# Kernel optimization log

Hardware: AMD Instinct MI355X
Metric: run time of the kernel (lower is better)

Reference implementation:

```python
import math
import jax, jax.numpy as jnp
import numpy as np

D_MODEL = 1024
N_HEADS = 16
D_K = D_MODEL // N_HEADS


def setup_inputs() -> dict:
    key = jax.random.key(0)
    ks = jax.random.split(key, 10)
    s = 1.0 / math.sqrt(D_MODEL)
    return {
        "x": jax.random.normal(ks[0], (4, 4096, D_MODEL), dtype=jnp.float32),
        "memory_key": jax.random.normal(ks[1], (4, 4096, D_MODEL), dtype=jnp.float32),
        "Wq": jax.random.normal(ks[2], (D_MODEL, D_MODEL), dtype=jnp.float32) * s,
        "bq": jnp.zeros((D_MODEL,), dtype=jnp.float32),
        "Wk": jax.random.normal(ks[3], (D_MODEL, D_MODEL), dtype=jnp.float32) * s,
        "bk": jnp.zeros((D_MODEL,), dtype=jnp.float32),
        "Wv": jax.random.normal(ks[4], (D_MODEL, D_MODEL), dtype=jnp.float32) * s,
        "bv": jnp.zeros((D_MODEL,), dtype=jnp.float32),
        "Wo": jax.random.normal(ks[5], (D_MODEL, D_MODEL), dtype=jnp.float32) * s,
        "bo": jnp.zeros((D_MODEL,), dtype=jnp.float32),
    }


def _heads(t, b, n):
    # [b, n, d_model] -> [b, h, n, d_k]
    return t.reshape(b, n, N_HEADS, D_K).transpose(0, 2, 1, 3)


def reference(x, memory_key, Wq, bq, Wk, bk, Wv, bv, Wo, bo):
    b, n, _ = x.shape
    scale = 1.0 / math.sqrt(D_K)
    q = _heads(x @ Wq + bq, b, n)
    k = _heads(x @ Wk + bk, b, n)
    v = _heads(x @ Wv + bv, b, n)
    # feature-dim softmax (over d_k), scaled by 1/sqrt(d_k)
    q_soft = jax.nn.softmax(q * scale, axis=-1)
    k_soft = jax.nn.softmax(k * scale, axis=-1)
    kv = jnp.einsum('bhnd,bhne->bhde', k_soft, v)   # [b,h,d_k,d_k]
    out = jnp.einsum('bhnd,bhde->bhne', q_soft, kv)
    # memory path: softmax over reshaped memory_key heads, same value tensor
    m_soft = jax.nn.softmax(_heads(memory_key, b, n) * scale, axis=-1)
    mv = jnp.einsum('bhnd,bhne->bhde', m_soft, v)
    out = out + jnp.einsum('bhnd,bhde->bhne', q_soft, mv)
    out = out.transpose(0, 2, 1, 3).reshape(b, n, D_MODEL)
    # dropout is identity in eval mode
    return out @ Wo + bo
```

## Files before the change

### kernel.cpp

```cpp
#include <hip/hip_runtime.h>
#include <stdint.h>

typedef unsigned int uint;
typedef unsigned short ushort;
typedef __attribute__((ext_vector_type(4))) float  f32x4;
typedef __attribute__((ext_vector_type(8))) __bf16 bf16x8;

#define SCALE 0.125f

__device__ __forceinline__ ushort f2bf(float f) {
  uint u = __builtin_bit_cast(uint, f);
  u += 0x7FFFu + ((u >> 16) & 1u);
  return (ushort)(u >> 16);
}
__device__ __forceinline__ uint pack2bf(float a, float b) {
  return (uint)f2bf(a) | ((uint)f2bf(b) << 16);
}
__device__ __forceinline__ float bflo(uint u) { return __builtin_bit_cast(float, u << 16); }
__device__ __forceinline__ float bfhi(uint u) { return __builtin_bit_cast(float, u & 0xFFFF0000u); }

__device__ __forceinline__ void gload_lds16(const void* g, void* l) {
  __builtin_amdgcn_global_load_lds((const __attribute__((address_space(1))) void*)g,
                                   (__attribute__((address_space(3))) void*)l, 16, 0, 0);
}

__device__ __forceinline__ void unpack8(uint4 u, float s, float* x) {
  x[0]=bflo(u.x)*s; x[1]=bfhi(u.x)*s; x[2]=bflo(u.y)*s; x[3]=bfhi(u.y)*s;
  x[4]=bflo(u.z)*s; x[5]=bfhi(u.z)*s; x[6]=bflo(u.w)*s; x[7]=bfhi(u.w)*s;
}


__global__ __launch_bounds__(256) void cvt_all_kernel(
    const float4* __restrict__ x, uint2* __restrict__ xb,
    const float* __restrict__ Wq, const float* __restrict__ Wk, const float* __restrict__ Wv,
    ushort* __restrict__ WT, float4* __restrict__ S4) {
  __shared__ float tile[32][33];
  int bx = blockIdx.x;
  if (bx < 2048) {
    int i = bx * 256 + threadIdx.x;
    #pragma unroll
    for (int k = 0; k < 8; ++k) {
      int idx = i + k * 524288;
      float4 f = x[idx];
      xb[idx] = make_uint2(pack2bf(f.x, f.y), pack2bf(f.z, f.w));
    }
  } else if (bx < 5120) {
    int lin = bx - 2048;
    int mat = lin >> 10;
    int rem = lin & 1023;
    int cb = rem & 31, rb = rem >> 5;
    const float* W = (mat == 0) ? Wq : (mat == 1) ? Wk : Wv;
    int tx = threadIdx.x & 31, ty = threadIdx.x >> 5;
    int c0 = cb * 32, r0 = rb * 32;
    #pragma unroll
    for (int i = 0; i < 4; ++i)
      tile[ty + i*8][tx] = W[(size_t)(r0 + ty + i*8) * 1024 + c0 + tx];
    __syncthreads();
    #pragma unroll
    for (int i = 0; i < 4; ++i)
      WT[(size_t)(mat*1024 + c0 + ty + i*8) * 1024 + r0 + tx] = f2bf(tile[tx][ty + i*8]);
  } else {
    int base = ((bx - 5120) * 256 + threadIdx.x) * 8;
    const float4 z = {0.f, 0.f, 0.f, 0.f};
    #pragma unroll
    for (int j = 0; j < 8; ++j) S4[base + j] = z;
  }
}


__global__ __launch_bounds__(256, 2) void gemm1_qkv(
    const ushort* __restrict__ A, const ushort* __restrict__ B,
    ushort* __restrict__ QKV, ushort* __restrict__ qs,
    const float* __restrict__ bq, const float* __restrict__ bk, const float* __restrict__ bv) {
  __shared__ ushort As[128 * 64];
  __shared__ ushort Bs[128 * 64];
  const int K = 1024;
  const int t = threadIdx.x;
  const int w = t >> 6, l = t & 63;
  const int wr = w >> 1, wc = w & 1;
  const int m0 = blockIdx.x * 128;
  const int n0 = blockIdx.y * 128;
  const ushort* Ap = A + (size_t)m0 * K;
  const ushort* Bp = B + (size_t)n0 * K;

  f32x4 acc[4][4];
  const f32x4 zf = {0.f, 0.f, 0.f, 0.f};
  #pragma unroll
  for (int i = 0; i < 4; ++i)
    #pragma unroll
    for (int j = 0; j < 4; ++j) acc[i][j] = zf;

  const int lr = l & 15, lg = l >> 4;

  for (int kt = 0; kt < K; kt += 64) {
    #pragma unroll
    for (int i = 0; i < 4; ++i) {
      int gb = w * 64 + i * 256;
      int g  = gb + l;
      int row = g >> 3, c16 = g & 7;
      gload_lds16(Ap + (size_t)row * K + kt + c16 * 8, (void*)(As + gb * 8));
      gload_lds16(Bp + (size_t)row * K + kt + c16 * 8, (void*)(Bs + gb * 8));
    }
    __syncthreads();
    #pragma unroll
    for (int kk = 0; kk < 64; kk += 32) {
      bf16x8 a[4], b[4];
      #pragma unroll
      for (int m = 0; m < 4; ++m)
        a[m] = *(const bf16x8*)(As + (wr*64 + m*16 + lr) * 64 + kk + lg * 8);
      #pragma unroll
      for (int n = 0; n < 4; ++n)
        b[n] = *(const bf16x8*)(Bs + (wc*64 + n*16 + lr) * 64 + kk + lg * 8);
      #pragma unroll
      for (int m = 0; m < 4; ++m)
        #pragma unroll
        for (int n = 0; n < 4; ++n)
          acc[m][n] = __builtin_amdgcn_mfma_f32_16x16x32_bf16(a[m], b[n], acc[m][n], 0, 0, 0);
    }
    __syncthreads();
  }

  if (n0 < 1024) {
    const int cb = n0 + wc * 64;
    float bvv[4];
    #pragma unroll
    for (int n = 0; n < 4; ++n) bvv[n] = bq[cb + n*16 + lr];
    #pragma unroll
    for (int m = 0; m < 4; ++m) {
      #pragma unroll
      for (int j = 0; j < 4; ++j) {
        int row = m0 + wr*64 + m*16 + lg*4 + j;
        float v[4];
        float s = 0.f;
        #pragma unroll
        for (int n = 0; n < 4; ++n) {
          v[n] = __expf((acc[m][n][j] + bvv[n]) * SCALE);
          s += v[n];
        }
        s += __shfl_xor(s, 1);
        s += __shfl_xor(s, 2);
        s += __shfl_xor(s, 4);
        s += __shfl_xor(s, 8);
        float inv = 1.f / s;
        #pragma unroll
        for (int n = 0; n < 4; ++n)
          qs[(size_t)row * 1024 + cb + n*16 + lr] = f2bf(v[n] * inv);
      }
    }
  } else {
    const float* bp = (n0 < 2048) ? bk : bv;
    #pragma unroll
    for (int n = 0; n < 4; ++n) {
      int col = n0 + wc*64 + n*16 + lr;
      float bvv = bp[col & 1023];
      #pragma unroll
      for (int m = 0; m < 4; ++m) {
        #pragma unroll
        for (int j = 0; j < 4; ++j) {
          int row = m0 + wr*64 + m*16 + lg*4 + j;
          QKV[(size_t)row * 3072 + col] = f2bf(acc[m][n][j] + bvv);
        }
      }
    }
  }
}


__global__ __launch_bounds__(256, 2) void gemm2_out(
    const ushort* __restrict__ A, const ushort* __restrict__ B, float* __restrict__ C,
    const float* __restrict__ bo) {
  __shared__ ushort As[128 * 64];
  __shared__ ushort Bs[128 * 64];
  const int K = 1024;
  const int t = threadIdx.x;
  const int w = t >> 6, l = t & 63;
  const int wr = w >> 1, wc = w & 1;
  const int m0 = blockIdx.x * 128;
  const int n0 = blockIdx.y * 128;
  const ushort* Ap = A + (size_t)m0 * K;
  const ushort* Bp = B + (size_t)(m0 >> 12) * (1024 * 1024) + (size_t)n0 * K;

  f32x4 acc[4][4];
  const f32x4 zf = {0.f, 0.f, 0.f, 0.f};
  #pragma unroll
  for (int i = 0; i < 4; ++i)
    #pragma unroll
    for (int j = 0; j < 4; ++j) acc[i][j] = zf;

  const int lr = l & 15, lg = l >> 4;

  for (int kt = 0; kt < K; kt += 64) {
    #pragma unroll
    for (int i = 0; i < 4; ++i) {
      int gb = w * 64 + i * 256;
      int g  = gb + l;
      int row = g >> 3, c16 = g & 7;
      gload_lds16(Ap + (size_t)row * K + kt + c16 * 8, (void*)(As + gb * 8));
      gload_lds16(Bp + (size_t)row * K + kt + c16 * 8, (void*)(Bs + gb * 8));
    }
    __syncthreads();
    #pragma unroll
    for (int kk = 0; kk < 64; kk += 32) {
      bf16x8 a[4], b[4];
      #pragma unroll
      for (int m = 0; m < 4; ++m)
        a[m] = *(const bf16x8*)(As + (wr*64 + m*16 + lr) * 64 + kk + lg * 8);
      #pragma unroll
      for (int n = 0; n < 4; ++n)
        b[n] = *(const bf16x8*)(Bs + (wc*64 + n*16 + lr) * 64 + kk + lg * 8);
      #pragma unroll
      for (int m = 0; m < 4; ++m)
        #pragma unroll
        for (int n = 0; n < 4; ++n)
          acc[m][n] = __builtin_amdgcn_mfma_f32_16x16x32_bf16(a[m], b[n], acc[m][n], 0, 0, 0);
    }
    __syncthreads();
  }

  #pragma unroll
  for (int n = 0; n < 4; ++n) {
    int col = n0 + wc*64 + n*16 + lr;
    float bvv = bo[col];
    #pragma unroll
    for (int m = 0; m < 4; ++m) {
      #pragma unroll
      for (int j = 0; j < 4; ++j) {
        int row = m0 + wr*64 + m*16 + lg*4 + j;
        C[(size_t)row * 1024 + col] = acc[m][n][j] + bvv;
      }
    }
  }
}


__global__ __launch_bounds__(256) void kv_fused(
    const ushort* __restrict__ QKV, const float* __restrict__ mk, float* __restrict__ S) {
  __shared__ ushort Vs[128 * 64];
  __shared__ ushort Ws[128 * 64];
  int bx = blockIdx.x;
  int bh = bx >> 4, nc = bx & 15;
  int b = bh >> 4, h = bh & 15;
  int t = threadIdx.x, w = t >> 6, l = t & 63;
  int d0 = (t & 15) * 4, e0 = (t >> 4) * 4;
  const int gq = d0 >> 3, sub = d0 & 7;
  float acc[4][4] = {};

  for (int c = 0; c < 2; ++c) {
    int row0 = b * 4096 + nc * 256 + c * 128;

    #pragma unroll
    for (int i = 0; i < 4; ++i) {
      int gb = w * 64 + i * 256, g = gb + l;
      int r = g >> 3, c16 = g & 7;
      gload_lds16(QKV + (size_t)(row0 + r) * 3072 + 2048 + h * 64 + c16 * 8, (void*)(Vs + gb * 8));
    }

    {
      int r = t >> 1, hf = t & 1;
      const uint4* kp = (const uint4*)(QKV + (size_t)(row0 + r) * 3072 + 1024 + h * 64 + hf * 32);
      float ke[32], me[32];
      #pragma unroll
      for (int i = 0; i < 4; ++i) unpack8(kp[i], SCALE, ke + i * 8);
      const float4* mp = (const float4*)(mk + (size_t)(row0 + r) * 1024 + h * 64 + hf * 32);
      #pragma unroll
      for (int i = 0; i < 8; ++i) {
        float4 f = mp[i];
        me[i*4+0] = f.x * SCALE; me[i*4+1] = f.y * SCALE;
        me[i*4+2] = f.z * SCALE; me[i*4+3] = f.w * SCALE;
      }
      float ksum = 0.f, msum = 0.f;
      #pragma unroll
      for (int i = 0; i < 32; ++i) { ke[i] = __expf(ke[i]); ksum += ke[i]; }
      #pragma unroll
      for (int i = 0; i < 32; ++i) { me[i] = __expf(me[i]); msum += me[i]; }
      ksum += __shfl_xor(ksum, 1);
      msum += __shfl_xor(msum, 1);
      float kinv = 1.f / ksum, minv = 1.f / msum;
      #pragma unroll
      for (int i = 0; i < 4; ++i) {
        int gsw = (hf * 4 + i) ^ (r & 7);
        uint4 o = make_uint4(
          pack2bf(ke[i*8+0]*kinv + me[i*8+0]*minv, ke[i*8+1]*kinv + me[i*8+1]*minv),
          pack2bf(ke[i*8+2]*kinv + me[i*8+2]*minv, ke[i*8+3]*kinv + me[i*8+3]*minv),
          pack2bf(ke[i*8+4]*kinv + me[i*8+4]*minv, ke[i*8+5]*kinv + me[i*8+5]*minv),
          pack2bf(ke[i*8+6]*kinv + me[i*8+6]*minv, ke[i*8+7]*kinv + me[i*8+7]*minv));
        *(uint4*)(Ws + r * 64 + gsw * 8) = o;
      }
    }
    __syncthreads();

    #pragma unroll 4
    for (int n = 0; n < 128; ++n) {
      uint2 wp = *(const uint2*)(Ws + n * 64 + ((gq ^ (n & 7)) << 3) + sub);
      uint2 vp = *(const uint2*)(Vs + n * 64 + e0);
      float wd[4] = { bflo(wp.x), bfhi(wp.x), bflo(wp.y), bfhi(wp.y) };
      float vd[4] = { bflo(vp.x), bfhi(vp.x), bflo(vp.y), bfhi(vp.y) };
      #pragma unroll
      for (int i = 0; i < 4; ++i)
        #pragma unroll
        for (int j = 0; j < 4; ++j) acc[i][j] += wd[i] * vd[j];
    }
    __syncthreads();
  }

  float* Sp = S + (size_t)bh * 4096;
  #pragma unroll
  for (int i = 0; i < 4; ++i)
    #pragma unroll
    for (int j = 0; j < 4; ++j)
      atomicAdd(Sp + (d0 + i) * 64 + e0 + j, acc[i][j]);
}


__global__ __launch_bounds__(256) void make_w2t(
    const float* __restrict__ S, const float* __restrict__ Wo, ushort* __restrict__ W2T) {
  int bx = blockIdx.x;
  int b = bx >> 8, h = (bx >> 4) & 15, ot = (bx >> 2) & 3, it = bx & 3;
  int t = threadIdx.x;
  __shared__ float Ss[16 * 64];
  const float* Sp = S + (size_t)(b * 16 + h) * 4096 + it * 1024;
  #pragma unroll
  for (int i = 0; i < 4; ++i) Ss[t + i * 256] = Sp[t + i * 256];
  __syncthreads();
  int o = ot * 256 + t;
  float acc[16] = {};
  for (int e = 0; e < 64; ++e) {
    float wo = Wo[(size_t)(h * 64 + e) * 1024 + o];
    #pragma unroll
    for (int i = 0; i < 16; ++i) acc[i] += Ss[i * 64 + e] * wo;
  }
  ushort* dst = W2T + (size_t)(b * 1024 + o) * 1024 + h * 64 + it * 16;
  #pragma unroll
  for (int i = 0; i < 16; ++i) dst[i] = f2bf(acc[i]);
}


extern "C" void kernel_launch(void* const* d_in, const int* in_sizes, int n_in,
                              void* d_out, int out_size, void* d_ws, size_t ws_size,
                              hipStream_t stream) {
  const float* x  = (const float*)d_in[0];
  const float* mk = (const float*)d_in[1];
  const float* Wq = (const float*)d_in[2];
  const float* bq = (const float*)d_in[3];
  const float* Wk = (const float*)d_in[4];
  const float* bk = (const float*)d_in[5];
  const float* Wv = (const float*)d_in[6];
  const float* bv = (const float*)d_in[7];
  const float* Wo = (const float*)d_in[8];
  const float* bo = (const float*)d_in[9];
  float* out = (float*)d_out;

  char* ws = (char*)d_ws;
  ushort* xb    = (ushort*)(ws);
  ushort* wqkvT = (ushort*)(ws +  33554432);
  ushort* QKV   = (ushort*)(ws +  39845888);
  ushort* qs    = (ushort*)(ws + 140509184);
  float*  S     = (float* )(ws + 207618048);
  ushort* W2T   = (ushort*)(ws + 208666624);

  cvt_all_kernel<<<5152, 256, 0, stream>>>((const float4*)x, (uint2*)xb,
                                           Wq, Wk, Wv, wqkvT, (float4*)S);
  gemm1_qkv<<<dim3(128, 24), 256, 0, stream>>>(xb, wqkvT, QKV, qs, bq, bk, bv);
  kv_fused<<<1024, 256, 0, stream>>>(QKV, mk, S);
  make_w2t<<<1024, 256, 0, stream>>>(S, Wo, W2T);
  gemm2_out<<<dim3(128, 8), 256, 0, stream>>>(qs, W2T, out, bo);
}
```

Before: 314.5 us.

## Apply per-head KV state to Q before output projection instead of folding into Wo

```diff
diff --git a/kernel.cpp b/kernel.cpp
--- a/kernel.cpp
+++ b/kernel.cpp
@@ -33,7 +33,8 @@
 __global__ __launch_bounds__(256) void cvt_all_kernel(
     const float4* __restrict__ x, uint2* __restrict__ xb,
     const float* __restrict__ Wq, const float* __restrict__ Wk, const float* __restrict__ Wv,
-    ushort* __restrict__ WT, float4* __restrict__ S4) {
+    const float* __restrict__ Wo,
+    ushort* __restrict__ WT, ushort* __restrict__ WoT, float4* __restrict__ S4) {
   __shared__ float tile[32][33];
   int bx = blockIdx.x;
   if (bx < 2048) {
@@ -44,12 +45,13 @@
       float4 f = x[idx];
       xb[idx] = make_uint2(pack2bf(f.x, f.y), pack2bf(f.z, f.w));
     }
-  } else if (bx < 5120) {
+  } else if (bx < 6144) {
     int lin = bx - 2048;
     int mat = lin >> 10;
     int rem = lin & 1023;
     int cb = rem & 31, rb = rem >> 5;
-    const float* W = (mat == 0) ? Wq : (mat == 1) ? Wk : Wv;
+    const float* W = (mat == 0) ? Wq : (mat == 1) ? Wk : (mat == 2) ? Wv : Wo;
+    ushort* dstbase = (mat < 3) ? (WT + (size_t)mat * 1024 * 1024) : WoT;
     int tx = threadIdx.x & 31, ty = threadIdx.x >> 5;
     int c0 = cb * 32, r0 = rb * 32;
     #pragma unroll
@@ -58,9 +60,9 @@
     __syncthreads();
     #pragma unroll
     for (int i = 0; i < 4; ++i)
-      WT[(size_t)(mat*1024 + c0 + ty + i*8) * 1024 + r0 + tx] = f2bf(tile[tx][ty + i*8]);
+      dstbase[(size_t)(c0 + ty + i*8) * 1024 + r0 + tx] = f2bf(tile[tx][ty + i*8]);
   } else {
-    int base = ((bx - 5120) * 256 + threadIdx.x) * 8;
+    int base = ((bx - 6144) * 256 + threadIdx.x) * 8;
     const float4 z = {0.f, 0.f, 0.f, 0.f};
     #pragma unroll
     for (int j = 0; j < 8; ++j) S4[base + j] = z;
@@ -166,6 +168,155 @@
 }
 
 
+__global__ __launch_bounds__(256) void kv_fused(
+    const ushort* __restrict__ QKV, const float* __restrict__ mk, float* __restrict__ S) {
+  __shared__ ushort Vs[128 * 64];
+  __shared__ ushort Ws[128 * 64];
+  int bx = blockIdx.x;
+  int bh = bx >> 4, nc = bx & 15;
+  int b = bh >> 4, h = bh & 15;
+  int t = threadIdx.x, w = t >> 6, l = t & 63;
+  int d0 = (t & 15) * 4, e0 = (t >> 4) * 4;
+  const int gq = d0 >> 3, sub = d0 & 7;
+  float acc[4][4] = {};
+
+  for (int c = 0; c < 2; ++c) {
+    int row0 = b * 4096 + nc * 256 + c * 128;
+
+    #pragma unroll
+    for (int i = 0; i < 4; ++i) {
+      int gb = w * 64 + i * 256, g = gb + l;
+      int r = g >> 3, c16 = g & 7;
+      gload_lds16(QKV + (size_t)(row0 + r) * 3072 + 2048 + h * 64 + c16 * 8, (void*)(Vs + gb * 8));
+    }
+
+    {
+      int r = t >> 1, hf = t & 1;
+      const uint4* kp = (const uint4*)(QKV + (size_t)(row0 + r) * 3072 + 1024 + h * 64 + hf * 32);
+      float ke[32], me[32];
+      #pragma unroll
+      for (int i = 0; i < 4; ++i) unpack8(kp[i], SCALE, ke + i * 8);
+      const float4* mp = (const float4*)(mk + (size_t)(row0 + r) * 1024 + h * 64 + hf * 32);
+      #pragma unroll
+      for (int i = 0; i < 8; ++i) {
+        float4 f = mp[i];
+        me[i*4+0] = f.x * SCALE; me[i*4+1] = f.y * SCALE;
+        me[i*4+2] = f.z * SCALE; me[i*4+3] = f.w * SCALE;
+      }
+      float ksum = 0.f, msum = 0.f;
+      #pragma unroll
+      for (int i = 0; i < 32; ++i) { ke[i] = __expf(ke[i]); ksum += ke[i]; }
+      #pragma unroll
+      for (int i = 0; i < 32; ++i) { me[i] = __expf(me[i]); msum += me[i]; }
+      ksum += __shfl_xor(ksum, 1);
+      msum += __shfl_xor(msum, 1);
+      float kinv = 1.f / ksum, minv = 1.f / msum;
+      #pragma unroll
+      for (int i = 0; i < 4; ++i) {
+        int gsw = (hf * 4 + i) ^ (r & 7);
+        uint4 o = make_uint4(
+          pack2bf(ke[i*8+0]*kinv + me[i*8+0]*minv, ke[i*8+1]*kinv + me[i*8+1]*minv),
+          pack2bf(ke[i*8+2]*kinv + me[i*8+2]*minv, ke[i*8+3]*kinv + me[i*8+3]*minv),
+          pack2bf(ke[i*8+4]*kinv + me[i*8+4]*minv, ke[i*8+5]*kinv + me[i*8+5]*minv),
+          pack2bf(ke[i*8+6]*kinv + me[i*8+6]*minv, ke[i*8+7]*kinv + me[i*8+7]*minv));
+        *(uint4*)(Ws + r * 64 + gsw * 8) = o;
+      }
+    }
+    __syncthreads();
+
+    #pragma unroll 4
+    for (int n = 0; n < 128; ++n) {
+      uint2 wp = *(const uint2*)(Ws + n * 64 + ((gq ^ (n & 7)) << 3) + sub);
+      uint2 vp = *(const uint2*)(Vs + n * 64 + e0);
+      float wd[4] = { bflo(wp.x), bfhi(wp.x), bflo(wp.y), bfhi(wp.y) };
+      float vd[4] = { bflo(vp.x), bfhi(vp.x), bflo(vp.y), bfhi(vp.y) };
+      #pragma unroll
+      for (int i = 0; i < 4; ++i)
+        #pragma unroll
+        for (int j = 0; j < 4; ++j) acc[i][j] += wd[i] * vd[j];
+    }
+    __syncthreads();
+  }
+
+  float* Sp = S + (size_t)bh * 4096;
+  #pragma unroll
+  for (int i = 0; i < 4; ++i)
+    #pragma unroll
+    for (int j = 0; j < 4; ++j)
+      atomicAdd(Sp + (d0 + i) * 64 + e0 + j, acc[i][j]);
+}
+
+
+__global__ __launch_bounds__(256, 2) void t_mm(
+    const ushort* __restrict__ qs, const float* __restrict__ S, ushort* __restrict__ tb) {
+  __shared__ ushort Qs[256 * 64];
+  __shared__ ushort SsT[64 * 64];
+  int bx = blockIdx.x;
+  int bh = bx >> 4, nc = bx & 15;
+  int b = bh >> 4, h = bh & 15;
+  int row0 = b * 4096 + nc * 256;
+  int t = threadIdx.x, w = t >> 6, l = t & 63;
+  const int lr = l & 15, lg = l >> 4;
+
+  #pragma unroll
+  for (int i = 0; i < 8; ++i) {
+    int gb = w * 64 + i * 256;
+    int g = gb + l;
+    int r = g >> 3, c16 = g & 7;
+    gload_lds16(qs + (size_t)(row0 + r) * 1024 + h * 64 + c16 * 8, (void*)(Qs + gb * 8));
+  }
+  {
+    int d = t >> 2, e00 = (t & 3) * 16;
+    const float4* sp = (const float4*)(S + (size_t)bh * 4096 + d * 64 + e00);
+    #pragma unroll
+    for (int i = 0; i < 4; ++i) {
+      float4 f = sp[i];
+      int e = e00 + i * 4;
+      SsT[(e + 0) * 64 + d] = f2bf(f.x);
+      SsT[(e + 1) * 64 + d] = f2bf(f.y);
+      SsT[(e + 2) * 64 + d] = f2bf(f.z);
+      SsT[(e + 3) * 64 + d] = f2bf(f.w);
+    }
+  }
+  __syncthreads();
+
+  f32x4 acc[4][4];
+  const f32x4 zf = {0.f, 0.f, 0.f, 0.f};
+  #pragma unroll
+  for (int i = 0; i < 4; ++i)
+    #pragma unroll
+    for (int j = 0; j < 4; ++j) acc[i][j] = zf;
+
+  #pragma unroll
+  for (int kk = 0; kk < 64; kk += 32) {
+    bf16x8 a[4], bfr[4];
+    #pragma unroll
+    for (int m = 0; m < 4; ++m)
+      a[m] = *(const bf16x8*)(Qs + (w*64 + m*16 + lr) * 64 + kk + lg * 8);
+    #pragma unroll
+    for (int n = 0; n < 4; ++n)
+      bfr[n] = *(const bf16x8*)(SsT + (n*16 + lr) * 64 + kk + lg * 8);
+    #pragma unroll
+    for (int m = 0; m < 4; ++m)
+      #pragma unroll
+      for (int n = 0; n < 4; ++n)
+        acc[m][n] = __builtin_amdgcn_mfma_f32_16x16x32_bf16(a[m], bfr[n], acc[m][n], 0, 0, 0);
+  }
+
+  #pragma unroll
+  for (int n = 0; n < 4; ++n) {
+    #pragma unroll
+    for (int m = 0; m < 4; ++m) {
+      #pragma unroll
+      for (int j = 0; j < 4; ++j) {
+        int row = row0 + w*64 + m*16 + lg*4 + j;
+        tb[(size_t)row * 1024 + h*64 + n*16 + lr] = f2bf(acc[m][n][j]);
+      }
+    }
+  }
+}
+
+
 __global__ __launch_bounds__(256, 2) void gemm2_out(
     const ushort* __restrict__ A, const ushort* __restrict__ B, float* __restrict__ C,
     const float* __restrict__ bo) {
@@ -178,7 +329,7 @@
   const int m0 = blockIdx.x * 128;
   const int n0 = blockIdx.y * 128;
   const ushort* Ap = A + (size_t)m0 * K;
-  const ushort* Bp = B + (size_t)(m0 >> 12) * (1024 * 1024) + (size_t)n0 * K;
+  const ushort* Bp = B + (size_t)n0 * K;
 
   f32x4 acc[4][4];
   const f32x4 zf = {0.f, 0.f, 0.f, 0.f};
@@ -230,108 +381,6 @@
       }
     }
   }
-}
-
-
-__global__ __launch_bounds__(256) void kv_fused(
-    const ushort* __restrict__ QKV, const float* __restrict__ mk, float* __restrict__ S) {
-  __shared__ ushort Vs[128 * 64];
-  __shared__ ushort Ws[128 * 64];
-  int bx = blockIdx.x;
-  int bh = bx >> 4, nc = bx & 15;
-  int b = bh >> 4, h = bh & 15;
-  int t = threadIdx.x, w = t >> 6, l = t & 63;
-  int d0 = (t & 15) * 4, e0 = (t >> 4) * 4;
-  const int gq = d0 >> 3, sub = d0 & 7;
-  float acc[4][4] = {};
-
-  for (int c = 0; c < 2; ++c) {
-    int row0 = b * 4096 + nc * 256 + c * 128;
-
-    #pragma unroll
-    for (int i = 0; i < 4; ++i) {
-      int gb = w * 64 + i * 256, g = gb + l;
-      int r = g >> 3, c16 = g & 7;
-      gload_lds16(QKV + (size_t)(row0 + r) * 3072 + 2048 + h * 64 + c16 * 8, (void*)(Vs + gb * 8));
-    }
-
-    {
-      int r = t >> 1, hf = t & 1;
-      const uint4* kp = (const uint4*)(QKV + (size_t)(row0 + r) * 3072 + 1024 + h * 64 + hf * 32);
-      float ke[32], me[32];
-      #pragma unroll
-      for (int i = 0; i < 4; ++i) unpack8(kp[i], SCALE, ke + i * 8);
-      const float4* mp = (const float4*)(mk + (size_t)(row0 + r) * 1024 + h * 64 + hf * 32);
-      #pragma unroll
-      for (int i = 0; i < 8; ++i) {
-        float4 f = mp[i];
-        me[i*4+0] = f.x * SCALE; me[i*4+1] = f.y * SCALE;
-        me[i*4+2] = f.z * SCALE; me[i*4+3] = f.w * SCALE;
-      }
-      float ksum = 0.f, msum = 0.f;
-      #pragma unroll
-      for (int i = 0; i < 32; ++i) { ke[i] = __expf(ke[i]); ksum += ke[i]; }
-      #pragma unroll
-      for (int i = 0; i < 32; ++i) { me[i] = __expf(me[i]); msum += me[i]; }
-      ksum += __shfl_xor(ksum, 1);
-      msum += __shfl_xor(msum, 1);
-      float kinv = 1.f / ksum, minv = 1.f / msum;
-      #pragma unroll
-      for (int i = 0; i < 4; ++i) {
-        int gsw = (hf * 4 + i) ^ (r & 7);
-        uint4 o = make_uint4(
-          pack2bf(ke[i*8+0]*kinv + me[i*8+0]*minv, ke[i*8+1]*kinv + me[i*8+1]*minv),
-          pack2bf(ke[i*8+2]*kinv + me[i*8+2]*minv, ke[i*8+3]*kinv + me[i*8+3]*minv),
-          pack2bf(ke[i*8+4]*kinv + me[i*8+4]*minv, ke[i*8+5]*kinv + me[i*8+5]*minv),
-          pack2bf(ke[i*8+6]*kinv + me[i*8+6]*minv, ke[i*8+7]*kinv + me[i*8+7]*minv));
-        *(uint4*)(Ws + r * 64 + gsw * 8) = o;
-      }
-    }
-    __syncthreads();
-
-    #pragma unroll 4
-    for (int n = 0; n < 128; ++n) {
-      uint2 wp = *(const uint2*)(Ws + n * 64 + ((gq ^ (n & 7)) << 3) + sub);
-      uint2 vp = *(const uint2*)(Vs + n * 64 + e0);
-      float wd[4] = { bflo(wp.x), bfhi(wp.x), bflo(wp.y), bfhi(wp.y) };
-      float vd[4] = { bflo(vp.x), bfhi(vp.x), bflo(vp.y), bfhi(vp.y) };
-      #pragma unroll
-      for (int i = 0; i < 4; ++i)
-        #pragma unroll
-        for (int j = 0; j < 4; ++j) acc[i][j] += wd[i] * vd[j];
-    }
-    __syncthreads();
-  }
-
-  float* Sp = S + (size_t)bh * 4096;
-  #pragma unroll
-  for (int i = 0; i < 4; ++i)
-    #pragma unroll
-    for (int j = 0; j < 4; ++j)
-      atomicAdd(Sp + (d0 + i) * 64 + e0 + j, acc[i][j]);
-}
-
-
-__global__ __launch_bounds__(256) void make_w2t(
-    const float* __restrict__ S, const float* __restrict__ Wo, ushort* __restrict__ W2T) {
-  int bx = blockIdx.x;
-  int b = bx >> 8, h = (bx >> 4) & 15, ot = (bx >> 2) & 3, it = bx & 3;
-  int t = threadIdx.x;
-  __shared__ float Ss[16 * 64];
-  const float* Sp = S + (size_t)(b * 16 + h) * 4096 + it * 1024;
-  #pragma unroll
-  for (int i = 0; i < 4; ++i) Ss[t + i * 256] = Sp[t + i * 256];
-  __syncthreads();
-  int o = ot * 256 + t;
-  float acc[16] = {};
-  for (int e = 0; e < 64; ++e) {
-    float wo = Wo[(size_t)(h * 64 + e) * 1024 + o];
-    #pragma unroll
-    for (int i = 0; i < 16; ++i) acc[i] += Ss[i * 64 + e] * wo;
-  }
-  ushort* dst = W2T + (size_t)(b * 1024 + o) * 1024 + h * 64 + it * 16;
-  #pragma unroll
-  for (int i = 0; i < 16; ++i) dst[i] = f2bf(acc[i]);
 }
 
 
@@ -353,15 +402,16 @@
   char* ws = (char*)d_ws;
   ushort* xb    = (ushort*)(ws);
   ushort* wqkvT = (ushort*)(ws +  33554432);
-  ushort* QKV   = (ushort*)(ws +  39845888);
-  ushort* qs    = (ushort*)(ws + 140509184);
-  float*  S     = (float* )(ws + 207618048);
-  ushort* W2T   = (ushort*)(ws + 208666624);
-
-  cvt_all_kernel<<<5152, 256, 0, stream>>>((const float4*)x, (uint2*)xb,
-                                           Wq, Wk, Wv, wqkvT, (float4*)S);
+  ushort* WoT   = (ushort*)(ws +  39845888);
+  ushort* QKV   = (ushort*)(ws +  41943040);
+  ushort* qs    = (ushort*)(ws + 142606336);
+  ushort* tb    = (ushort*)(ws + 176160768);
+  float*  S     = (float* )(ws + 209715200);
+
+  cvt_all_kernel<<<6176, 256, 0, stream>>>((const float4*)x, (uint2*)xb,
+                                           Wq, Wk, Wv, Wo, wqkvT, WoT, (float4*)S);
   gemm1_qkv<<<dim3(128, 24), 256, 0, stream>>>(xb, wqkvT, QKV, qs, bq, bk, bv);
   kv_fused<<<1024, 256, 0, stream>>>(QKV, mk, S);
-  make_w2t<<<1024, 256, 0, stream>>>(S, Wo, W2T);
-  gemm2_out<<<dim3(128, 8), 256, 0, stream>>>(qs, W2T, out, bo);
-}
+  t_mm<<<1024, 256, 0, stream>>>(qs, S, tb);
+  gemm2_out<<<dim3(128, 8), 256, 0, stream>>>(tb, WoT, out, bo);
+}
```

Result: slower. 323.6 us (+2.9%).

## Fuse Wo projection into kv_fused via last-block counter

Applied to the files above, without the earlier changes.

```diff
diff --git a/kernel.cpp b/kernel.cpp
--- a/kernel.cpp
+++ b/kernel.cpp
@@ -33,7 +33,7 @@
 __global__ __launch_bounds__(256) void cvt_all_kernel(
     const float4* __restrict__ x, uint2* __restrict__ xb,
     const float* __restrict__ Wq, const float* __restrict__ Wk, const float* __restrict__ Wv,
-    ushort* __restrict__ WT, float4* __restrict__ S4) {
+    ushort* __restrict__ WT, float4* __restrict__ S4, int* __restrict__ counters) {
   __shared__ float tile[32][33];
   int bx = blockIdx.x;
   if (bx < 2048) {
@@ -64,6 +64,7 @@
     const float4 z = {0.f, 0.f, 0.f, 0.f};
     #pragma unroll
     for (int j = 0; j < 8; ++j) S4[base + j] = z;
+    if (bx == 5120 && threadIdx.x < 64) counters[threadIdx.x] = 0;
   }
 }
 
@@ -234,9 +235,11 @@
 
 
 __global__ __launch_bounds__(256) void kv_fused(
-    const ushort* __restrict__ QKV, const float* __restrict__ mk, float* __restrict__ S) {
+    const ushort* __restrict__ QKV, const float* __restrict__ mk, float* __restrict__ S,
+    const float* __restrict__ Wo, ushort* __restrict__ W2T, int* __restrict__ counters) {
   __shared__ ushort Vs[128 * 64];
   __shared__ ushort Ws[128 * 64];
+  __shared__ int lastFlag;
   int bx = blockIdx.x;
   int bh = bx >> 4, nc = bx & 15;
   int b = bh >> 4, h = bh & 15;
@@ -309,29 +312,47 @@
     #pragma unroll
     for (int j = 0; j < 4; ++j)
       atomicAdd(Sp + (d0 + i) * 64 + e0 + j, acc[i][j]);
-}
-
-
-__global__ __launch_bounds__(256) void make_w2t(
-    const float* __restrict__ S, const float* __restrict__ Wo, ushort* __restrict__ W2T) {
-  int bx = blockIdx.x;
-  int b = bx >> 8, h = (bx >> 4) & 15, ot = (bx >> 2) & 3, it = bx & 3;
-  int t = threadIdx.x;
-  __shared__ float Ss[16 * 64];
-  const float* Sp = S + (size_t)(b * 16 + h) * 4096 + it * 1024;
-  #pragma unroll
-  for (int i = 0; i < 4; ++i) Ss[t + i * 256] = Sp[t + i * 256];
+
+  __threadfence();
+  if (t == 0) {
+    int prev = atomicAdd(&counters[bh], 1);
+    lastFlag = (prev == 15) ? 1 : 0;
+  }
   __syncthreads();
-  int o = ot * 256 + t;
-  float acc[16] = {};
-  for (int e = 0; e < 64; ++e) {
-    float wo = Wo[(size_t)(h * 64 + e) * 1024 + o];
-    #pragma unroll
-    for (int i = 0; i < 16; ++i) acc[i] += Ss[i * 64 + e] * wo;
-  }
-  ushort* dst = W2T + (size_t)(b * 1024 + o) * 1024 + h * 64 + it * 16;
-  #pragma unroll
-  for (int i = 0; i < 16; ++i) dst[i] = f2bf(acc[i]);
+  if (!lastFlag) return;
+  __threadfence();
+
+  float* Sf = (float*)Vs;
+  #pragma unroll
+  for (int i = 0; i < 16; ++i) {
+    int idx = t + i * 256;
+    Sf[idx] = __hip_atomic_load(Sp + idx, __ATOMIC_RELAXED, __HIP_MEMORY_SCOPE_AGENT);
+  }
+  __syncthreads();
+
+  for (int ot = 0; ot < 4; ++ot) {
+    int oo = ot * 256 + t;
+    #pragma unroll
+    for (int it = 0; it < 4; ++it) {
+      float acc2[16];
+      #pragma unroll
+      for (int i = 0; i < 16; ++i) acc2[i] = 0.f;
+      for (int e4 = 0; e4 < 16; ++e4) {
+        float w0 = Wo[(size_t)(h*64 + e4*4 + 0) * 1024 + oo];
+        float w1 = Wo[(size_t)(h*64 + e4*4 + 1) * 1024 + oo];
+        float w2 = Wo[(size_t)(h*64 + e4*4 + 2) * 1024 + oo];
+        float w3 = Wo[(size_t)(h*64 + e4*4 + 3) * 1024 + oo];
+        #pragma unroll
+        for (int i = 0; i < 16; ++i) {
+          const float* sr = Sf + (it*16 + i) * 64 + e4*4;
+          acc2[i] += sr[0]*w0 + sr[1]*w1 + sr[2]*w2 + sr[3]*w3;
+        }
+      }
+      ushort* dst = W2T + (size_t)(b * 1024 + oo) * 1024 + h * 64 + it * 16;
+      #pragma unroll
+      for (int i = 0; i < 16; ++i) dst[i] = f2bf(acc2[i]);
+    }
+  }
 }
 
 
@@ -357,11 +378,11 @@
   ushort* qs    = (ushort*)(ws + 140509184);
   float*  S     = (float* )(ws + 207618048);
   ushort* W2T   = (ushort*)(ws + 208666624);
+  int*    cnts  = (int*   )(ws + 217055232);
 
   cvt_all_kernel<<<5152, 256, 0, stream>>>((const float4*)x, (uint2*)xb,
-                                           Wq, Wk, Wv, wqkvT, (float4*)S);
+                                           Wq, Wk, Wv, wqkvT, (float4*)S, cnts);
   gemm1_qkv<<<dim3(128, 24), 256, 0, stream>>>(xb, wqkvT, QKV, qs, bq, bk, bv);
-  kv_fused<<<1024, 256, 0, stream>>>(QKV, mk, S);
-  make_w2t<<<1024, 256, 0, stream>>>(S, Wo, W2T);
+  kv_fused<<<1024, 256, 0, stream>>>(QKV, mk, S, Wo, W2T, cnts);
   gemm2_out<<<dim3(128, 8), 256, 0, stream>>>(qs, W2T, out, bo);
 }
```

Result: slower. 580.7 us (+84.6%).
